# Performance work log

Measured on AMD Instinct MI355X. Metric: run time of the kernel, lower is better.

The kernel has to match this reference:

```python
import jax, jax.numpy as jnp
import numpy as np

HIDDEN = 1024
ATT = 512

def _xavier(key, shape):
    fan_in, fan_out = shape[0], shape[1]
    bound = float(np.sqrt(6.0 / (fan_in + fan_out)))
    return jax.random.uniform(key, shape, jnp.float32, -bound, bound)

def setup_inputs() -> dict:
    key = jax.random.key(0)
    ks = jax.random.split(key, 7)
    B, P = 256, 196
    spatial_image = jax.random.normal(ks[0], (B, P, HIDDEN), jnp.float32)
    decoder_out = jax.random.normal(ks[1], (B, HIDDEN), jnp.float32)
    st = jax.random.normal(ks[2], (B, HIDDEN), jnp.float32)
    # weights stored as (in_dim, out_dim); math identical to torch Linear(x @ W.T)
    W_cnn = _xavier(ks[3], (HIDDEN, ATT))
    W_dec = _xavier(ks[4], (HIDDEN, ATT))
    W_sen = _xavier(ks[5], (HIDDEN, ATT))
    W_att = _xavier(ks[6], (ATT, 1))
    return {"spatial_image": spatial_image, "decoder_out": decoder_out, "st": st,
            "W_cnn": W_cnn, "W_dec": W_dec, "W_sen": W_sen, "W_att": W_att}

def reference(spatial_image, decoder_out, st, W_cnn, W_dec, W_sen, W_att):
    # dropout in eval mode (identity)
    cnn_out = jnp.einsum('bph,ha->bpa', spatial_image, W_cnn)   # (B,P,A)
    dec_out = decoder_out @ W_dec                                # (B,A)
    addition = jnp.tanh(cnn_out + dec_out[:, None, :])           # (B,P,A)
    zt = jnp.einsum('bpa,a->bp', addition, W_att[:, 0])          # (B,P)
    alpha_t = jax.nn.softmax(zt, axis=1)                         # (B,P)
    ct = jnp.einsum('bph,bp->bh', spatial_image, alpha_t)        # (B,H)
    sen = jnp.tanh(dec_out + st @ W_sen)                         # (B,A)
    out = sen @ W_att                                            # (B,1)
    concat = jnp.concatenate([zt, out], axis=1)                  # (B,P+1)
    alpha_hat = jax.nn.softmax(concat, axis=1)
    beta_t = alpha_hat[:, -1:]                                   # (B,1)
    c_hat = beta_t * st + (1.0 - beta_t) * ct                    # (B,H)
    return (alpha_t, beta_t, c_hat)
```

## Files before the change

### kernel.cpp

```cpp
#include <hip/hip_runtime.h>
#include <hip/hip_bf16.h>

#define BATCH   256
#define NP      196
#define HIDDEN  1024
#define ATT     512
#define M_TOTAL (BATCH * NP)
#define BM 128
#define BN 256
#define BK 32
#define MT_TILES (M_TOTAL / BM)
#define NB_TILES (ATT / BN)

typedef __attribute__((ext_vector_type(8))) short bf16x8v;
typedef __attribute__((ext_vector_type(4))) float f32x4;

__device__ inline unsigned short f2bf(float x) {
    unsigned int u = __float_as_uint(x);
    u += 0x7fffu + ((u >> 16) & 1u);
    return (unsigned short)(u >> 16);
}

__device__ __forceinline__ unsigned int pk2bf(float lo, float hi) {
    unsigned int r;
    asm("v_cvt_pk_bf16_f32 %0, %1, %2" : "=v"(r) : "v"(lo), "v"(hi));
    return r;
}

__device__ inline float fast_tanh(float x) {
    float e = __expf(2.0f * x);
    return 1.0f - 2.0f / (e + 1.0f);
}

__device__ __forceinline__ void glds16(const void* gsrc, void* ldst) {
    __builtin_amdgcn_global_load_lds(
        (const __attribute__((address_space(1))) unsigned int*)gsrc,
        (__attribute__((address_space(3))) unsigned int*)ldst,
        16, 0, 0);
}

__global__ void k0_arrange(const float* __restrict__ Wc, unsigned short* __restrict__ Wt) {
    int g = blockIdx.x * 256 + threadIdx.x;
    int nb    = g >> 15;
    int rem   = g & 32767;
    int kt    = rem >> 10;
    int chunk = (rem >> 8) & 3;
    int n     = rem & 255;
    int col   = nb * 256 + n;
    int kb    = kt * 32 + chunk * 8;
    unsigned short v[8];
#pragma unroll
    for (int j = 0; j < 8; ++j) v[j] = f2bf(Wc[(size_t)(kb + j) * ATT + col]);
    uint4 pk;
    pk.x = (unsigned int)v[0] | ((unsigned int)v[1] << 16);
    pk.y = (unsigned int)v[2] | ((unsigned int)v[3] << 16);
    pk.z = (unsigned int)v[4] | ((unsigned int)v[5] << 16);
    pk.w = (unsigned int)v[6] | ((unsigned int)v[7] << 16);
    *(uint4*)(Wt + (size_t)g * 8) = pk;
}

__global__ void k1_small(const float* __restrict__ dec_in, const float* __restrict__ st,
                         const float* __restrict__ Wdec,  const float* __restrict__ Wsen,
                         float* __restrict__ dec_out, float* __restrict__ stw) {
    const float* X = blockIdx.z ? st   : dec_in;
    const float* W = blockIdx.z ? Wsen : Wdec;
    float*       O = blockIdx.z ? stw  : dec_out;
    int ci = threadIdx.x & 31;
    int c0 = blockIdx.x * 128 + ci * 4;
    int b  = blockIdx.y * 8 + (threadIdx.x >> 5);
    const float* x = X + (size_t)b * HIDDEN;
    float4 acc = {0.f, 0.f, 0.f, 0.f};
    for (int k = 0; k < HIDDEN; k += 4) {
#pragma unroll
        for (int kk = 0; kk < 4; ++kk) {
            float4 w = *(const float4*)(W + (size_t)(k + kk) * ATT + c0);
            float a = x[k + kk];
            acc.x += a * w.x; acc.y += a * w.y; acc.z += a * w.z; acc.w += a * w.w;
        }
    }
    *(float4*)(O + (size_t)b * ATT + c0) = acc;
}

__global__ void __launch_bounds__(512, 4)
k2_fused_gemm(const float* __restrict__ A, const unsigned short* __restrict__ Wt,
              const float* __restrict__ dec, const float* __restrict__ Watt,
              float* __restrict__ ztp) {
    __shared__ __align__(16) unsigned short Abuf[4 * 128 * 8];
    __shared__ __align__(16) unsigned short Bbuf[4 * 256 * 8];
    __shared__ float zred[128 * 4];

    const int tid = threadIdx.x;
    const int w  = tid >> 6;
    const int l  = tid & 63;
    const int lg = l >> 4, ll = l & 15;
    const int wr = w >> 2, wc = w & 3;

    const int bid = (int)blockIdx.x;
    const int swz = (bid & 7) * 98 + (bid >> 3);
    const int mt = swz >> 1, nb = swz & 1;
    const int r0 = mt * BM;
    const int c0 = nb * BN;

    f32x4 acc[4][4];
#pragma unroll
    for (int m = 0; m < 4; ++m)
#pragma unroll
        for (int n = 0; n < 4; ++n) acc[m][n] = (f32x4){0.f, 0.f, 0.f, 0.f};

    const int arow = tid >> 2;
    const int ach  = tid & 3;
    const float* aptr = A + (size_t)(r0 + arow) * HIDDEN + ach * 8;
    unsigned short* aslot = Abuf + (ach * 128 + arow) * 8;

    const size_t wt_base = (size_t)nb * 32 * 8192;
    const char* bsrc0 = (const char*)(Wt + wt_base) + (w * 2 + 0) * 1024 + l * 16;
    const char* bsrc1 = (const char*)(Wt + wt_base) + (w * 2 + 1) * 1024 + l * 16;
    char* bdst0 = (char*)Bbuf + (w * 2 + 0) * 1024 + l * 16;
    char* bdst1 = (char*)Bbuf + (w * 2 + 1) * 1024 + l * 16;

    float4 a0 = *(const float4*)(aptr);
    float4 a1 = *(const float4*)(aptr + 4);

    for (int kt = 0; kt < 32; ++kt) {
        __syncthreads();

        glds16(bsrc0 + kt * 16384, bdst0);
        glds16(bsrc1 + kt * 16384, bdst1);

        uint4 ap;
        ap.x = pk2bf(a0.x, a0.y);
        ap.y = pk2bf(a0.z, a0.w);
        ap.z = pk2bf(a1.x, a1.y);
        ap.w = pk2bf(a1.z, a1.w);
        *(uint4*)aslot = ap;

        __syncthreads();

        if (kt < 31) {
            a0 = *(const float4*)(aptr + (kt + 1) * 32);
            a1 = *(const float4*)(aptr + (kt + 1) * 32 + 4);
        }

        bf16x8v af[4], bfr[4];
#pragma unroll
        for (int m = 0; m < 4; ++m)
            af[m] = *(const bf16x8v*)(Abuf + ((lg * 128 + wr * 64 + m * 16 + ll) << 3));
#pragma unroll
        for (int n = 0; n < 4; ++n)
            bfr[n] = *(const bf16x8v*)(Bbuf + ((lg * 256 + wc * 64 + n * 16 + ll) << 3));
#pragma unroll
        for (int m = 0; m < 4; ++m)
#pragma unroll
            for (int n = 0; n < 4; ++n)
                acc[m][n] = __builtin_amdgcn_mfma_f32_16x16x32_bf16(af[m], bfr[n], acc[m][n], 0, 0, 0);
    }

    const int clocal = wc * 64 + ll;
    float watt[4];
#pragma unroll
    for (int n = 0; n < 4; ++n) watt[n] = Watt[c0 + clocal + n * 16];

#pragma unroll
    for (int m = 0; m < 4; ++m) {
#pragma unroll
        for (int j = 0; j < 4; ++j) {
            int rl = wr * 64 + m * 16 + lg * 4 + j;
            int rowg = r0 + rl;
            int b = rowg / NP;
            const float* db = dec + (size_t)b * ATT + c0;
            float s = 0.f;
#pragma unroll
            for (int n = 0; n < 4; ++n)
                s += fast_tanh(acc[m][n][j] + db[clocal + n * 16]) * watt[n];
            s += __shfl_xor(s, 1);
            s += __shfl_xor(s, 2);
            s += __shfl_xor(s, 4);
            s += __shfl_xor(s, 8);
            if (ll == 0) zred[rl * 4 + wc] = s;
        }
    }
    __syncthreads();
    if (tid < 128) {
        float t = zred[tid * 4] + zred[tid * 4 + 1] + zred[tid * 4 + 2] + zred[tid * 4 + 3];
        ztp[(size_t)nb * M_TOTAL + r0 + tid] = t;
    }
}

__global__ void k3_softmax(const float* __restrict__ dec, const float* __restrict__ stw,
                           const float* __restrict__ Watt, const float* __restrict__ ztp,
                           float* __restrict__ out, float* __restrict__ beta_ws) {
    int b = blockIdx.x;
    int t = threadIdx.x;
    __shared__ float red[256];

    float p = 0.f;
#pragma unroll
    for (int c = t; c < ATT; c += 256)
        p += fast_tanh(dec[(size_t)b * ATT + c] + stw[(size_t)b * ATT + c]) * Watt[c];
    red[t] = p;
    __syncthreads();
    for (int s = 128; s > 0; s >>= 1) { if (t < s) red[t] += red[t + s]; __syncthreads(); }
    float outv = red[0];
    __syncthreads();

    float z = -1e30f;
    if (t < NP) z = ztp[b * NP + t] + ztp[M_TOTAL + b * NP + t];
    red[t] = z;
    __syncthreads();
    for (int s = 128; s > 0; s >>= 1) { if (t < s) red[t] = fmaxf(red[t], red[t + s]); __syncthreads(); }
    float m1 = red[0];
    __syncthreads();

    float e = (t < NP) ? __expf(z - m1) : 0.f;
    red[t] = e;
    __syncthreads();
    for (int s = 128; s > 0; s >>= 1) { if (t < s) red[t] += red[t + s]; __syncthreads(); }
    float s1 = red[0];

    if (t < NP) out[b * NP + t] = e / s1;

    if (t == 0) {
        float m2 = fmaxf(m1, outv);
        float s2 = s1 * __expf(m1 - m2) + __expf(outv - m2);
        float beta = __expf(outv - m2) / s2;
        out[M_TOTAL + b] = beta;
        beta_ws[b] = beta;
    }
}

__global__ void k4_ct(const float* __restrict__ spatial, const float* __restrict__ alpha,
                      float* __restrict__ ctp) {
    int q = blockIdx.x;
    int b = blockIdx.y;
    int t = threadIdx.x;
    __shared__ float al[49];
    if (t < 49) al[t] = alpha[b * NP + q * 49 + t];
    __syncthreads();
    const float* sp = spatial + (size_t)b * NP * HIDDEN + (size_t)q * 49 * HIDDEN + t * 4;
    float4 acc = {0.f, 0.f, 0.f, 0.f};
#pragma unroll 7
    for (int p = 0; p < 49; ++p) {
        float4 v = *(const float4*)(sp + (size_t)p * HIDDEN);
        float a = al[p];
        acc.x += a * v.x; acc.y += a * v.y; acc.z += a * v.z; acc.w += a * v.w;
    }
    *(float4*)(ctp + ((size_t)q * BATCH + b) * HIDDEN + t * 4) = acc;
}

__global__ void k5_chat(const float* __restrict__ st, const float* __restrict__ ctp,
                        const float* __restrict__ beta, float* __restrict__ chat) {
    int g = blockIdx.x * 256 + threadIdx.x;
    int b = g >> 8;
    int h0 = (g & 255) * 4;
    float be = beta[b];
    float4 s = *(const float4*)(st + (size_t)b * HIDDEN + h0);
    float4 c = {0.f, 0.f, 0.f, 0.f};
#pragma unroll
    for (int q = 0; q < 4; ++q) {
        float4 v = *(const float4*)(ctp + ((size_t)q * BATCH + b) * HIDDEN + h0);
        c.x += v.x; c.y += v.y; c.z += v.z; c.w += v.w;
    }
    float4 o;
    o.x = be * s.x + (1.f - be) * c.x;
    o.y = be * s.y + (1.f - be) * c.y;
    o.z = be * s.z + (1.f - be) * c.z;
    o.w = be * s.w + (1.f - be) * c.w;
    *(float4*)(chat + (size_t)b * HIDDEN + h0) = o;
}

extern "C" void kernel_launch(void* const* d_in, const int* in_sizes, int n_in,
                              void* d_out, int out_size, void* d_ws, size_t ws_size,
                              hipStream_t stream) {
    const float* spatial = (const float*)d_in[0];
    const float* decoder = (const float*)d_in[1];
    const float* st      = (const float*)d_in[2];
    const float* Wcnn    = (const float*)d_in[3];
    const float* Wdec    = (const float*)d_in[4];
    const float* Wsen    = (const float*)d_in[5];
    const float* Watt    = (const float*)d_in[6];
    float* out = (float*)d_out;

    char* ws = (char*)d_ws;
    unsigned short* Wt = (unsigned short*)(ws + 0);
    float* ztp  = (float*)(ws + 1048576);
    float* dec  = (float*)(ws + 1449984);
    float* stw  = (float*)(ws + 1974272);
    float* beta = (float*)(ws + 2498560);
    float* ctp  = (float*)(ws + 2499584);

    k0_arrange<<<256, 256, 0, stream>>>(Wcnn, Wt);
    k1_small<<<dim3(4, 32, 2), 256, 0, stream>>>(decoder, st, Wdec, Wsen, dec, stw);
    k2_fused_gemm<<<MT_TILES * NB_TILES, 512, 0, stream>>>(spatial, Wt, dec, Watt, ztp);
    k3_softmax<<<256, 256, 0, stream>>>(dec, stw, Watt, ztp, out, beta);
    k4_ct<<<dim3(4, 256), 256, 0, stream>>>(spatial, out, ctp);
    k5_chat<<<256, 256, 0, stream>>>(st, ctp, beta, out + M_TOTAL + BATCH);
}
```

Baseline: 186.2 us.

## Double-buffer LDS tiles and prefetch A two steps ahead in fused GEMM

Switches the A and B shared-memory tiles to two buffers, so the next B tile is loaded by global-to-LDS copies and the next A tile is converted and stored while the current tile feeds the MFMAs. The main loop now has one barrier per iteration instead of two, uses manual waitcnt, and prefetches A registers two iterations ahead. This aims to hide global load latency behind compute. The cost is doubled LDS use, which may lower occupancy under the 512x4 launch bounds, and more registers, plus fragile hand-written vmcnt accounting.

Result: faster. 173.1 us (-7.0%).

```diff
diff --git a/kernel.cpp b/kernel.cpp
--- a/kernel.cpp
+++ b/kernel.cpp
@@ -85,8 +85,8 @@
 k2_fused_gemm(const float* __restrict__ A, const unsigned short* __restrict__ Wt,
               const float* __restrict__ dec, const float* __restrict__ Watt,
               float* __restrict__ ztp) {
-    __shared__ __align__(16) unsigned short Abuf[4 * 128 * 8];
-    __shared__ __align__(16) unsigned short Bbuf[4 * 256 * 8];
+    __shared__ __align__(16) unsigned short Abuf[2][4 * 128 * 8];
+    __shared__ __align__(16) unsigned short Bbuf[2][4 * 256 * 8];
     __shared__ float zred[128 * 4];
 
     const int tid = threadIdx.x;
@@ -110,44 +110,75 @@
     const int arow = tid >> 2;
     const int ach  = tid & 3;
     const float* aptr = A + (size_t)(r0 + arow) * HIDDEN + ach * 8;
-    unsigned short* aslot = Abuf + (ach * 128 + arow) * 8;
+    const int aslot = (ach * 128 + arow) * 8;
 
     const size_t wt_base = (size_t)nb * 32 * 8192;
-    const char* bsrc0 = (const char*)(Wt + wt_base) + (w * 2 + 0) * 1024 + l * 16;
-    const char* bsrc1 = (const char*)(Wt + wt_base) + (w * 2 + 1) * 1024 + l * 16;
-    char* bdst0 = (char*)Bbuf + (w * 2 + 0) * 1024 + l * 16;
-    char* bdst1 = (char*)Bbuf + (w * 2 + 1) * 1024 + l * 16;
-
-    float4 a0 = *(const float4*)(aptr);
-    float4 a1 = *(const float4*)(aptr + 4);
-
-    for (int kt = 0; kt < 32; ++kt) {
-        __syncthreads();
-
-        glds16(bsrc0 + kt * 16384, bdst0);
-        glds16(bsrc1 + kt * 16384, bdst1);
-
+    const char* bsrc0 = (const char*)(Wt + wt_base) + w * 2048 + l * 16;
+    const char* bsrc1 = bsrc0 + 1024;
+    const int boff0 = w * 2048 + l * 16;
+    const int boff1 = boff0 + 1024;
+
+    glds16(bsrc0, (char*)Bbuf[0] + boff0);
+    glds16(bsrc1, (char*)Bbuf[0] + boff1);
+    float4 t0a = *(const float4*)(aptr);
+    float4 t0b = *(const float4*)(aptr + 4);
+    float4 aN0 = *(const float4*)(aptr + 32);
+    float4 aN1 = *(const float4*)(aptr + 36);
+    {
         uint4 ap;
-        ap.x = pk2bf(a0.x, a0.y);
-        ap.y = pk2bf(a0.z, a0.w);
-        ap.z = pk2bf(a1.x, a1.y);
-        ap.w = pk2bf(a1.z, a1.w);
-        *(uint4*)aslot = ap;
-
-        __syncthreads();
-
-        if (kt < 31) {
-            a0 = *(const float4*)(aptr + (kt + 1) * 32);
-            a1 = *(const float4*)(aptr + (kt + 1) * 32 + 4);
-        }
+        ap.x = pk2bf(t0a.x, t0a.y);
+        ap.y = pk2bf(t0a.z, t0a.w);
+        ap.z = pk2bf(t0b.x, t0b.y);
+        ap.w = pk2bf(t0b.z, t0b.w);
+        *(uint4*)(Abuf[0] + aslot) = ap;
+    }
+    asm volatile("s_waitcnt vmcnt(2) lgkmcnt(0)" ::: "memory");
+    __builtin_amdgcn_s_barrier();
+
+    for (int kt = 0; kt < 31; ++kt) {
+        const int cur = kt & 1;
+        const int nxt = cur ^ 1;
+
+        glds16(bsrc0 + (size_t)(kt + 1) * 16384, (char*)Bbuf[nxt] + boff0);
+        glds16(bsrc1 + (size_t)(kt + 1) * 16384, (char*)Bbuf[nxt] + boff1);
+
+        const int kt2 = (kt + 2 < 32) ? (kt + 2) : 31;
+        float4 aM0 = *(const float4*)(aptr + kt2 * 32);
+        float4 aM1 = *(const float4*)(aptr + kt2 * 32 + 4);
 
         bf16x8v af[4], bfr[4];
 #pragma unroll
         for (int m = 0; m < 4; ++m)
-            af[m] = *(const bf16x8v*)(Abuf + ((lg * 128 + wr * 64 + m * 16 + ll) << 3));
+            af[m] = *(const bf16x8v*)(Abuf[cur] + ((lg * 128 + wr * 64 + m * 16 + ll) << 3));
 #pragma unroll
         for (int n = 0; n < 4; ++n)
-            bfr[n] = *(const bf16x8v*)(Bbuf + ((lg * 256 + wc * 64 + n * 16 + ll) << 3));
+            bfr[n] = *(const bf16x8v*)(Bbuf[cur] + ((lg * 256 + wc * 64 + n * 16 + ll) << 3));
+#pragma unroll
+        for (int m = 0; m < 4; ++m)
+#pragma unroll
+            for (int n = 0; n < 4; ++n)
+                acc[m][n] = __builtin_amdgcn_mfma_f32_16x16x32_bf16(af[m], bfr[n], acc[m][n], 0, 0, 0);
+
+        uint4 ap;
+        ap.x = pk2bf(aN0.x, aN0.y);
+        ap.y = pk2bf(aN0.z, aN0.w);
+        ap.z = pk2bf(aN1.x, aN1.y);
+        ap.w = pk2bf(aN1.z, aN1.w);
+        *(uint4*)(Abuf[nxt] + aslot) = ap;
+        aN0 = aM0; aN1 = aM1;
+
+        asm volatile("s_waitcnt vmcnt(2) lgkmcnt(0)" ::: "memory");
+        __builtin_amdgcn_s_barrier();
+    }
+
+    {
+        bf16x8v af[4], bfr[4];
+#pragma unroll
+        for (int m = 0; m < 4; ++m)
+            af[m] = *(const bf16x8v*)(Abuf[1] + ((lg * 128 + wr * 64 + m * 16 + ll) << 3));
+#pragma unroll
+        for (int n = 0; n < 4; ++n)
+            bfr[n] = *(const bf16x8v*)(Bbuf[1] + ((lg * 256 + wc * 64 + n * 16 + ll) << 3));
 #pragma unroll
         for (int m = 0; m < 4; ++m)
 #pragma unroll
```

## Triple-buffer GEMM with direct-to-LDS fp32 A loads and narrower N tiles

Applied to the files above, without the earlier changes.

Restructures the fused cnn GEMM. A and B tiles now load through global_load_lds into a three-stage LDS ring, with partial vmcnt waits so loads overlap the MFMA work. A stays fp32 in LDS with an XOR swizzle and is converted to bf16 at fragment-read time, replacing the old register-staged conversion and double barrier. N tiles shrink from 256 to 128 columns, which doubles the block count and gives four partial z buffers that the softmax kernel now sums. The cost is more A reloads across N tiles, double the LDS bytes for A, and a bigger workspace layout.

After: 191.9 us. 3.1% more time.

```diff
diff --git a/kernel.cpp b/kernel.cpp
--- a/kernel.cpp
+++ b/kernel.cpp
@@ -7,10 +7,9 @@
 #define ATT     512
 #define M_TOTAL (BATCH * NP)
 #define BM 128
-#define BN 256
-#define BK 32
+#define BN 128
+#define NB_TILES (ATT / BN)
 #define MT_TILES (M_TOTAL / BM)
-#define NB_TILES (ATT / BN)
 
 typedef __attribute__((ext_vector_type(8))) short bf16x8v;
 typedef __attribute__((ext_vector_type(4))) float f32x4;
@@ -41,12 +40,11 @@
 
 __global__ void k0_arrange(const float* __restrict__ Wc, unsigned short* __restrict__ Wt) {
     int g = blockIdx.x * 256 + threadIdx.x;
-    int nb    = g >> 15;
-    int rem   = g & 32767;
-    int kt    = rem >> 10;
-    int chunk = (rem >> 8) & 3;
-    int n     = rem & 255;
-    int col   = nb * 256 + n;
+    int nb    = g >> 14;
+    int kt    = (g >> 9) & 31;
+    int chunk = (g >> 7) & 3;
+    int colp  = g & 127;
+    int col   = nb * 128 + ((colp - chunk * 4) & 127);
     int kb    = kt * 32 + chunk * 8;
     unsigned short v[8];
 #pragma unroll
@@ -85,75 +83,92 @@
 k2_fused_gemm(const float* __restrict__ A, const unsigned short* __restrict__ Wt,
               const float* __restrict__ dec, const float* __restrict__ Watt,
               float* __restrict__ ztp) {
-    __shared__ __align__(16) unsigned short Abuf[4 * 128 * 8];
-    __shared__ __align__(16) unsigned short Bbuf[4 * 256 * 8];
-    __shared__ float zred[128 * 4];
+    __shared__ __align__(16) char lds[3 * 24576];
+    __shared__ float zred[256];
 
     const int tid = threadIdx.x;
     const int w  = tid >> 6;
     const int l  = tid & 63;
     const int lg = l >> 4, ll = l & 15;
-    const int wr = w >> 2, wc = w & 3;
+    const int wr = w >> 1, wc = w & 1;
 
     const int bid = (int)blockIdx.x;
-    const int swz = (bid & 7) * 98 + (bid >> 3);
-    const int mt = swz >> 1, nb = swz & 1;
+    const int swz = (bid & 7) * 196 + (bid >> 3);
+    const int mt = swz >> 2, nb = swz & 3;
     const int r0 = mt * BM;
     const int c0 = nb * BN;
 
-    f32x4 acc[4][4];
-#pragma unroll
-    for (int m = 0; m < 4; ++m)
+    f32x4 acc[2][4];
+#pragma unroll
+    for (int m = 0; m < 2; ++m)
 #pragma unroll
         for (int n = 0; n < 4; ++n) acc[m][n] = (f32x4){0.f, 0.f, 0.f, 0.f};
 
-    const int arow = tid >> 2;
-    const int ach  = tid & 3;
-    const float* aptr = A + (size_t)(r0 + arow) * HIDDEN + ach * 8;
-    unsigned short* aslot = Abuf + (ach * 128 + arow) * 8;
-
-    const size_t wt_base = (size_t)nb * 32 * 8192;
-    const char* bsrc0 = (const char*)(Wt + wt_base) + (w * 2 + 0) * 1024 + l * 16;
-    const char* bsrc1 = (const char*)(Wt + wt_base) + (w * 2 + 1) * 1024 + l * 16;
-    char* bdst0 = (char*)Bbuf + (w * 2 + 0) * 1024 + l * 16;
-    char* bdst1 = (char*)Bbuf + (w * 2 + 1) * 1024 + l * 16;
-
-    float4 a0 = *(const float4*)(aptr);
-    float4 a1 = *(const float4*)(aptr + 4);
-
-    for (int kt = 0; kt < 32; ++kt) {
-        __syncthreads();
-
-        glds16(bsrc0 + kt * 16384, bdst0);
-        glds16(bsrc1 + kt * 16384, bdst1);
-
-        uint4 ap;
-        ap.x = pk2bf(a0.x, a0.y);
-        ap.y = pk2bf(a0.z, a0.w);
-        ap.z = pk2bf(a1.x, a1.y);
-        ap.w = pk2bf(a1.z, a1.w);
-        *(uint4*)aslot = ap;
-
-        __syncthreads();
-
-        if (kt < 31) {
-            a0 = *(const float4*)(aptr + (kt + 1) * 32);
-            a1 = *(const float4*)(aptr + (kt + 1) * 32 + 4);
-        }
-
-        bf16x8v af[4], bfr[4];
-#pragma unroll
-        for (int m = 0; m < 4; ++m)
-            af[m] = *(const bf16x8v*)(Abuf + ((lg * 128 + wr * 64 + m * 16 + ll) << 3));
-#pragma unroll
-        for (int n = 0; n < 4; ++n)
-            bfr[n] = *(const bf16x8v*)(Bbuf + ((lg * 256 + wc * 64 + n * 16 + ll) << 3));
-#pragma unroll
-        for (int m = 0; m < 4; ++m)
-#pragma unroll
-            for (int n = 0; n < 4; ++n)
-                acc[m][n] = __builtin_amdgcn_mfma_f32_16x16x32_bf16(af[m], bfr[n], acc[m][n], 0, 0, 0);
-    }
+    char* ldsb = (char*)lds;
+
+    const int row_d0 = (tid >> 3);
+    const int row_d1 = 64 + (tid >> 3);
+    const int sp = tid & 7;
+    const float* asrc0 = A + (size_t)(r0 + row_d0) * HIDDEN + (sp ^ (row_d0 & 7)) * 4;
+    const float* asrc1 = A + (size_t)(r0 + row_d1) * HIDDEN + (sp ^ (row_d1 & 7)) * 4;
+    const char* bsrc = (const char*)Wt + (size_t)nb * 262144 + tid * 16;
+
+#define STAGE(kt, q) do {                                                     \
+    glds16(asrc0 + (kt) * 32, ldsb + (q) * 24576 + tid * 16);                 \
+    glds16(asrc1 + (kt) * 32, ldsb + (q) * 24576 + 8192 + tid * 16);          \
+    glds16(bsrc + (size_t)(kt) * 8192, ldsb + (q) * 24576 + 16384 + tid * 16);\
+} while (0)
+
+#define COMPUTE(q) do {                                                       \
+    const char* Ab = ldsb + (q) * 24576;                                      \
+    const char* Bb = Ab + 16384;                                              \
+    bf16x8v af[2];                                                            \
+    _Pragma("unroll")                                                         \
+    for (int m = 0; m < 2; ++m) {                                             \
+        int rl = wr * 32 + m * 16 + ll;                                       \
+        int base = rl * 128;                                                  \
+        f32x4 lo = *(const f32x4*)(Ab + base + (((lg * 2 + 0) ^ (rl & 7)) << 4)); \
+        f32x4 hi = *(const f32x4*)(Ab + base + (((lg * 2 + 1) ^ (rl & 7)) << 4)); \
+        uint4 u;                                                              \
+        u.x = pk2bf(lo.x, lo.y); u.y = pk2bf(lo.z, lo.w);                     \
+        u.z = pk2bf(hi.x, hi.y); u.w = pk2bf(hi.z, hi.w);                     \
+        af[m] = *(bf16x8v*)&u;                                                \
+    }                                                                         \
+    bf16x8v bfr[4];                                                           \
+    _Pragma("unroll")                                                         \
+    for (int n = 0; n < 4; ++n) {                                             \
+        int colp = ((wc * 64 + n * 16 + ll) + lg * 4) & 127;                  \
+        bfr[n] = *(const bf16x8v*)(Bb + lg * 2048 + colp * 16);               \
+    }                                                                         \
+    __builtin_amdgcn_s_setprio(1);                                            \
+    _Pragma("unroll")                                                         \
+    for (int m = 0; m < 2; ++m)                                               \
+        _Pragma("unroll")                                                     \
+        for (int n = 0; n < 4; ++n)                                           \
+            acc[m][n] = __builtin_amdgcn_mfma_f32_16x16x32_bf16(af[m], bfr[n], acc[m][n], 0, 0, 0); \
+    __builtin_amdgcn_s_setprio(0);                                            \
+} while (0)
+
+#define WAIT3 asm volatile("s_waitcnt vmcnt(3) lgkmcnt(0)" ::: "memory")
+#define BAR   __builtin_amdgcn_s_barrier()
+
+    STAGE(0, 0);
+    STAGE(1, 1);
+
+    for (int tb = 0; tb < 30; tb += 3) {
+        WAIT3; BAR; STAGE(tb + 2, 2); COMPUTE(0);
+        WAIT3; BAR; STAGE(tb + 3, 0); COMPUTE(1);
+        WAIT3; BAR; STAGE(tb + 4, 1); COMPUTE(2);
+    }
+    WAIT3; BAR; COMPUTE(0);
+    asm volatile("s_waitcnt vmcnt(0) lgkmcnt(0)" ::: "memory");
+    BAR;
+    COMPUTE(1);
+
+#undef STAGE
+#undef COMPUTE
+#undef WAIT3
+#undef BAR
 
     const int clocal = wc * 64 + ll;
     float watt[4];
@@ -161,10 +176,10 @@
     for (int n = 0; n < 4; ++n) watt[n] = Watt[c0 + clocal + n * 16];
 
 #pragma unroll
-    for (int m = 0; m < 4; ++m) {
+    for (int m = 0; m < 2; ++m) {
 #pragma unroll
         for (int j = 0; j < 4; ++j) {
-            int rl = wr * 64 + m * 16 + lg * 4 + j;
+            int rl = wr * 32 + m * 16 + lg * 4 + j;
             int rowg = r0 + rl;
             int b = rowg / NP;
             const float* db = dec + (size_t)b * ATT + c0;
@@ -176,12 +191,12 @@
             s += __shfl_xor(s, 2);
             s += __shfl_xor(s, 4);
             s += __shfl_xor(s, 8);
-            if (ll == 0) zred[rl * 4 + wc] = s;
+            if (ll == 0) zred[rl * 2 + wc] = s;
         }
     }
     __syncthreads();
     if (tid < 128) {
-        float t = zred[tid * 4] + zred[tid * 4 + 1] + zred[tid * 4 + 2] + zred[tid * 4 + 3];
+        float t = zred[tid * 2] + zred[tid * 2 + 1];
         ztp[(size_t)nb * M_TOTAL + r0 + tid] = t;
     }
 }
@@ -204,7 +219,10 @@
     __syncthreads();
 
     float z = -1e30f;
-    if (t < NP) z = ztp[b * NP + t] + ztp[M_TOTAL + b * NP + t];
+    if (t < NP) {
+        z = ztp[b * NP + t] + ztp[M_TOTAL + b * NP + t]
+          + ztp[2 * M_TOTAL + b * NP + t] + ztp[3 * M_TOTAL + b * NP + t];
+    }
     red[t] = z;
     __syncthreads();
     for (int s = 128; s > 0; s >>= 1) { if (t < s) red[t] = fmaxf(red[t], red[t + s]); __syncthreads(); }
@@ -283,10 +301,10 @@
     char* ws = (char*)d_ws;
     unsigned short* Wt = (unsigned short*)(ws + 0);
     float* ztp  = (float*)(ws + 1048576);
-    float* dec  = (float*)(ws + 1449984);
-    float* stw  = (float*)(ws + 1974272);
-    float* beta = (float*)(ws + 2498560);
-    float* ctp  = (float*)(ws + 2499584);
+    float* dec  = (float*)(ws + 1851392);
+    float* stw  = (float*)(ws + 2375680);
+    float* beta = (float*)(ws + 2899968);
+    float* ctp  = (float*)(ws + 2901504);
 
     k0_arrange<<<256, 256, 0, stream>>>(Wcnn, Wt);
     k1_small<<<dim3(4, 32, 2), 256, 0, stream>>>(decoder, st, Wdec, Wsen, dec, stw);
```

## Double-buffer fused GEMM with larger 256x256x64 tiles and XOR-swizzled LDS

Applied to the files above, without the earlier changes.

Restructures the main GEMM kernel into a double-buffered LDS pipeline, loading the next K-step of A and B while MFMAs run on the current one. The M tile grows from 128 to 256 rows and BK from 32 to 64, and the weight pre-arrangement and A writes use an XOR swizzle to avoid LDS bank conflicts. The aim is to hide global-load latency, halve the barrier count and raise data reuse per block. In exchange, LDS use rises to 128KB plus the reduction buffer and registers roughly double, so occupancy drops (launch bounds go from 4 to 2) and fewer, larger blocks may leave CUs underfilled.

New measurement: 201.6 us. 1.08x slower.

```diff
diff --git a/kernel.cpp b/kernel.cpp
--- a/kernel.cpp
+++ b/kernel.cpp
@@ -6,11 +6,12 @@
 #define HIDDEN  1024
 #define ATT     512
 #define M_TOTAL (BATCH * NP)
-#define BM 128
+#define BM 256
 #define BN 256
-#define BK 32
+#define BK 64
+#define NB_TILES (ATT / BN)
 #define MT_TILES (M_TOTAL / BM)
-#define NB_TILES (ATT / BN)
+#define KSTEPS   (HIDDEN / BK)
 
 typedef __attribute__((ext_vector_type(8))) short bf16x8v;
 typedef __attribute__((ext_vector_type(4))) float f32x4;
@@ -41,16 +42,16 @@
 
 __global__ void k0_arrange(const float* __restrict__ Wc, unsigned short* __restrict__ Wt) {
     int g = blockIdx.x * 256 + threadIdx.x;
-    int nb    = g >> 15;
-    int rem   = g & 32767;
-    int kt    = rem >> 10;
-    int chunk = (rem >> 8) & 3;
-    int n     = rem & 255;
-    int col   = nb * 256 + n;
-    int kb    = kt * 32 + chunk * 8;
+    int nb  = g >> 15;
+    int ks  = (g >> 11) & 15;
+    int col = (g >> 3) & 255;
+    int cp  = g & 7;
+    int c   = cp ^ (col & 7);
+    int kb  = ks * 64 + c * 8;
+    int colg = nb * 256 + col;
     unsigned short v[8];
 #pragma unroll
-    for (int j = 0; j < 8; ++j) v[j] = f2bf(Wc[(size_t)(kb + j) * ATT + col]);
+    for (int j = 0; j < 8; ++j) v[j] = f2bf(Wc[(size_t)(kb + j) * ATT + colg]);
     uint4 pk;
     pk.x = (unsigned int)v[0] | ((unsigned int)v[1] << 16);
     pk.y = (unsigned int)v[2] | ((unsigned int)v[3] << 16);
@@ -81,13 +82,12 @@
     *(float4*)(O + (size_t)b * ATT + c0) = acc;
 }
 
-__global__ void __launch_bounds__(512, 4)
+__global__ void __launch_bounds__(512, 2)
 k2_fused_gemm(const float* __restrict__ A, const unsigned short* __restrict__ Wt,
               const float* __restrict__ dec, const float* __restrict__ Watt,
               float* __restrict__ ztp) {
-    __shared__ __align__(16) unsigned short Abuf[4 * 128 * 8];
-    __shared__ __align__(16) unsigned short Bbuf[4 * 256 * 8];
-    __shared__ float zred[128 * 4];
+    __shared__ __align__(16) char lds[131072];
+    __shared__ float zred[1024];
 
     const int tid = threadIdx.x;
     const int w  = tid >> 6;
@@ -96,64 +96,111 @@
     const int wr = w >> 2, wc = w & 3;
 
     const int bid = (int)blockIdx.x;
-    const int swz = (bid & 7) * 98 + (bid >> 3);
+    const int swz = (bid & 7) * 49 + (bid >> 3);
     const int mt = swz >> 1, nb = swz & 1;
     const int r0 = mt * BM;
     const int c0 = nb * BN;
 
-    f32x4 acc[4][4];
-#pragma unroll
-    for (int m = 0; m < 4; ++m)
+    char* Abuf0 = lds;
+    char* Abuf1 = lds + 32768;
+    char* Bbuf0 = lds + 65536;
+    char* Bbuf1 = lds + 98304;
+
+    f32x4 acc[8][4];
+#pragma unroll
+    for (int m = 0; m < 8; ++m)
 #pragma unroll
         for (int n = 0; n < 4; ++n) acc[m][n] = (f32x4){0.f, 0.f, 0.f, 0.f};
 
-    const int arow = tid >> 2;
-    const int ach  = tid & 3;
-    const float* aptr = A + (size_t)(r0 + arow) * HIDDEN + ach * 8;
-    unsigned short* aslot = Abuf + (ach * 128 + arow) * 8;
-
-    const size_t wt_base = (size_t)nb * 32 * 8192;
-    const char* bsrc0 = (const char*)(Wt + wt_base) + (w * 2 + 0) * 1024 + l * 16;
-    const char* bsrc1 = (const char*)(Wt + wt_base) + (w * 2 + 1) * 1024 + l * 16;
-    char* bdst0 = (char*)Bbuf + (w * 2 + 0) * 1024 + l * 16;
-    char* bdst1 = (char*)Bbuf + (w * 2 + 1) * 1024 + l * 16;
-
-    float4 a0 = *(const float4*)(aptr);
-    float4 a1 = *(const float4*)(aptr + 4);
-
-    for (int kt = 0; kt < 32; ++kt) {
-        __syncthreads();
-
-        glds16(bsrc0 + kt * 16384, bdst0);
-        glds16(bsrc1 + kt * 16384, bdst1);
-
-        uint4 ap;
-        ap.x = pk2bf(a0.x, a0.y);
-        ap.y = pk2bf(a0.z, a0.w);
-        ap.z = pk2bf(a1.x, a1.y);
-        ap.w = pk2bf(a1.z, a1.w);
-        *(uint4*)aslot = ap;
-
-        __syncthreads();
-
-        if (kt < 31) {
-            a0 = *(const float4*)(aptr + (kt + 1) * 32);
-            a1 = *(const float4*)(aptr + (kt + 1) * 32 + 4);
-        }
-
-        bf16x8v af[4], bfr[4];
-#pragma unroll
-        for (int m = 0; m < 4; ++m)
-            af[m] = *(const bf16x8v*)(Abuf + ((lg * 128 + wr * 64 + m * 16 + ll) << 3));
-#pragma unroll
-        for (int n = 0; n < 4; ++n)
-            bfr[n] = *(const bf16x8v*)(Bbuf + ((lg * 256 + wc * 64 + n * 16 + ll) << 3));
-#pragma unroll
-        for (int m = 0; m < 4; ++m)
-#pragma unroll
-            for (int n = 0; n < 4; ++n)
-                acc[m][n] = __builtin_amdgcn_mfma_f32_16x16x32_bf16(af[m], bfr[n], acc[m][n], 0, 0, 0);
-    }
+    const int arow_b = tid >> 4;
+    const int k4 = tid & 15;
+    const float* asrc = A + (size_t)(r0 + arow_b) * HIDDEN + k4 * 4;
+    const int aw_off = ((((k4 >> 1) ^ (arow_b & 7)) << 4) | ((k4 & 1) << 3));
+
+    const char* bsrc = (const char*)Wt + (size_t)nb * (KSTEPS * 32768) + tid * 16;
+
+    float4 av[8];
+
+#define ALOAD(t) do {                                                          \
+    _Pragma("unroll")                                                          \
+    for (int j = 0; j < 8; ++j)                                                \
+        av[j] = *(const float4*)(asrc + (size_t)j * 32 * HIDDEN + (t) * 64);   \
+} while (0)
+
+#define BGLDS(t, Bb) do {                                                      \
+    _Pragma("unroll")                                                          \
+    for (int q = 0; q < 4; ++q)                                                \
+        glds16(bsrc + (size_t)(t) * 32768 + q * 8192, (Bb) + q * 8192 + tid * 16); \
+} while (0)
+
+#define AWRITE(Ab) do {                                                        \
+    _Pragma("unroll")                                                          \
+    for (int j = 0; j < 8; ++j) {                                              \
+        int row = arow_b + 32 * j;                                             \
+        uint2 u;                                                               \
+        u.x = pk2bf(av[j].x, av[j].y);                                         \
+        u.y = pk2bf(av[j].z, av[j].w);                                         \
+        *(uint2*)((Ab) + row * 128 + aw_off) = u;                              \
+    }                                                                          \
+} while (0)
+
+#define COMPUTE(Ab, Bb) do {                                                   \
+    _Pragma("unroll")                                                          \
+    for (int kk = 0; kk < 2; ++kk) {                                           \
+        bf16x8v bfr[4];                                                        \
+        _Pragma("unroll")                                                      \
+        for (int n = 0; n < 4; ++n) {                                          \
+            int coll = wc * 64 + n * 16 + ll;                                  \
+            bfr[n] = *(const bf16x8v*)((Bb) + coll * 128 +                     \
+                                       (((kk * 4 + lg) ^ (ll & 7)) << 4));     \
+        }                                                                      \
+        _Pragma("unroll")                                                      \
+        for (int m = 0; m < 8; ++m) {                                          \
+            int rowl = wr * 128 + m * 16 + ll;                                 \
+            bf16x8v af = *(const bf16x8v*)((Ab) + rowl * 128 +                 \
+                                           (((kk * 4 + lg) ^ (ll & 7)) << 4)); \
+            _Pragma("unroll")                                                  \
+            for (int n = 0; n < 4; ++n)                                        \
+                acc[m][n] = __builtin_amdgcn_mfma_f32_16x16x32_bf16(           \
+                    af, bfr[n], acc[m][n], 0, 0, 0);                           \
+        }                                                                      \
+    }                                                                          \
+} while (0)
+
+#define SYNC do {                                                              \
+    asm volatile("s_waitcnt vmcnt(0) lgkmcnt(0)" ::: "memory");                \
+    __builtin_amdgcn_s_barrier();                                              \
+} while (0)
+
+    ALOAD(0);
+    BGLDS(0, Bbuf0);
+    AWRITE(Abuf0);
+    SYNC;
+
+    for (int tb = 0; tb < 14; tb += 2) {
+        ALOAD(tb + 1);
+        BGLDS(tb + 1, Bbuf1);
+        COMPUTE(Abuf0, Bbuf0);
+        AWRITE(Abuf1);
+        SYNC;
+        ALOAD(tb + 2);
+        BGLDS(tb + 2, Bbuf0);
+        COMPUTE(Abuf1, Bbuf1);
+        AWRITE(Abuf0);
+        SYNC;
+    }
+    ALOAD(15);
+    BGLDS(15, Bbuf1);
+    COMPUTE(Abuf0, Bbuf0);
+    AWRITE(Abuf1);
+    SYNC;
+    COMPUTE(Abuf1, Bbuf1);
+
+#undef ALOAD
+#undef BGLDS
+#undef AWRITE
+#undef COMPUTE
+#undef SYNC
 
     const int clocal = wc * 64 + ll;
     float watt[4];
@@ -161,10 +208,10 @@
     for (int n = 0; n < 4; ++n) watt[n] = Watt[c0 + clocal + n * 16];
 
 #pragma unroll
-    for (int m = 0; m < 4; ++m) {
+    for (int m = 0; m < 8; ++m) {
 #pragma unroll
         for (int j = 0; j < 4; ++j) {
-            int rl = wr * 64 + m * 16 + lg * 4 + j;
+            int rl = wr * 128 + m * 16 + lg * 4 + j;
             int rowg = r0 + rl;
             int b = rowg / NP;
             const float* db = dec + (size_t)b * ATT + c0;
@@ -180,7 +227,7 @@
         }
     }
     __syncthreads();
-    if (tid < 128) {
+    if (tid < 256) {
         float t = zred[tid * 4] + zred[tid * 4 + 1] + zred[tid * 4 + 2] + zred[tid * 4 + 3];
         ztp[(size_t)nb * M_TOTAL + r0 + tid] = t;
     }
```
